# Optimization experiments

Hardware: AMD Instinct MI355X
Metric: run time of the kernel (lower is better)

The kernel has to match this reference:

```python
import jax, jax.numpy as jnp
import numpy as np
from jax import lax

E, S, Q, FEAT, HID, WAY = 4000, 25, 75, 64, 128, 5
ITERS = 10
LR = 0.01


def setup_inputs() -> dict:
    key = jax.random.key(0)
    ks = jax.random.split(key, 7)
    u = lambda k, shape, fan_in: jax.random.uniform(k, shape, jnp.float32, -1.0, 1.0) / jnp.sqrt(float(fan_in))
    return {
        "query_feat": jax.random.normal(ks[0], (E, Q, FEAT), jnp.float32),
        "support_feat": jax.random.normal(ks[1], (E, S, FEAT), jnp.float32),
        "support_targets": jax.random.randint(ks[2], (E, S), 0, WAY, jnp.int32),
        "W1": u(ks[3], (E, HID, FEAT), FEAT),
        "b1": u(ks[4], (E, HID), FEAT),
        "W2": u(ks[5], (E, WAY, HID), HID),
        "b2": u(ks[6], (E, WAY), HID),
    }


def _mlp(p, x):
    h = jax.nn.relu(x @ p["W1"].T + p["b1"])
    return h @ p["W2"].T + p["b2"]


def _train_episode(W1, b1, W2, b2, s_feat, s_tgt):
    params = {"W1": W1, "b1": b1, "W2": W2, "b2": b2}

    def loss_fn(p):
        logp = jax.nn.log_softmax(_mlp(p, s_feat), axis=-1)  # [S, WAY]
        return -jnp.mean(jnp.take_along_axis(logp, s_tgt[:, None], axis=1))

    def step(p, _):
        g = jax.grad(loss_fn)(p)
        return jax.tree.map(lambda a, b: a - LR * b, p, g), None

    params, _ = lax.scan(step, params, None, length=ITERS)
    return params


def reference(query_feat, support_feat, support_targets, W1, b1, W2, b2):
    # support features are detached in the original torch code
    support_feat = lax.stop_gradient(support_feat)

    def per_episode(q, s, t, w1, c1, w2, c2):
        p = _train_episode(w1, c1, w2, c2, s, t)
        return _mlp(p, q)  # [Q, WAY]

    out = jax.vmap(per_episode)(query_feat, support_feat, support_targets, W1, b1, W2, b2)
    return out.reshape(-1, out.shape[-1])  # torch.cat over episodes -> [E*Q, WAY]
```

## Files before the change

kernel.cpp:

```cpp
#include <hip/hip_runtime.h>

#define S 25
#define Q 75
#define FEAT 64
#define HID 128
#define WAY 5
#define NITERS 10
#define LR 0.01f
#define THREADS 256
#define HPAD 132

__device__ __forceinline__ int w1word(int j, int k) {
    const int q = k >> 2;
    return j * FEAT + ((q & 8) << 2) + (((q ^ j) & 7) << 2) + (k & 3);
}

__global__ __launch_bounds__(THREADS, 2)
void episode_kernel(const float* __restrict__ qf,
                    const float* __restrict__ sf,
                    const int* __restrict__ st,
                    const float* __restrict__ W1g,
                    const float* __restrict__ b1g,
                    const float* __restrict__ W2g,
                    const float* __restrict__ b2g,
                    float* __restrict__ outg)
{
    __shared__ __align__(16) float sW1[HID * FEAT];
    __shared__ __align__(16) float sW2[WAY * HID];
    __shared__ __align__(16) float sX[S * FEAT];
    __shared__ __align__(16) float sH[S * HPAD];
    __shared__ __align__(16) float sDh[S * HPAD];
    __shared__ __align__(16) float sDl[S * 8];
    __shared__ float sb1[HID];
    __shared__ float sb2[8];
    __shared__ int sTgt[S];

    const int e = blockIdx.x;
    const int t = threadIdx.x;

    const float* eQ  = qf  + (size_t)e * Q * FEAT;
    const float* eS  = sf  + (size_t)e * S * FEAT;
    const int*   eT  = st  + (size_t)e * S;
    const float* eW1 = W1g + (size_t)e * HID * FEAT;
    const float* eb1 = b1g + (size_t)e * HID;
    const float* eW2 = W2g + (size_t)e * WAY * HID;
    const float* eb2 = b2g + (size_t)e * WAY;
    float*       eO  = outg + (size_t)e * Q * WAY;

    for (int f = t; f < HID * FEAT; f += THREADS)
        sW1[w1word(f >> 6, f & 63)] = eW1[f];
    for (int f = t; f < S * FEAT; f += THREADS) sX[f] = eS[f];
    for (int f = t; f < WAY * HID; f += THREADS) sW2[f] = eW2[f];
    if (t < HID) sb1[t] = eb1[t];
    if (t < WAY) sb2[t] = eb2[t];
    if (t < S)   sTgt[t] = eT[t];
    __syncthreads();

    const int j   = t & (HID - 1);
    const int grp = t >> 7;
    const int i0  = grp * 12;
    const int jl = t & 63;
    const int k0 = (t >> 6) << 4;

    for (int iter = 0; iter < NITERS; ++iter) {
        {
            float acc[13];
            const float bv = sb1[j];
            #pragma unroll
            for (int r = 0; r < 13; ++r) acc[r] = bv;
            for (int qd = 0; qd < 16; ++qd) {
                const float4 w = *(const float4*)&sW1[j * FEAT + ((qd & 8) << 2) + (((qd ^ j) & 7) << 2)];
                const float* xp = &sX[i0 * FEAT + (qd << 2)];
                #pragma unroll
                for (int r = 0; r < 13; ++r) {
                    const float4 s = *(const float4*)&xp[r * FEAT];
                    acc[r] = fmaf(w.x, s.x, acc[r]);
                    acc[r] = fmaf(w.y, s.y, acc[r]);
                    acc[r] = fmaf(w.z, s.z, acc[r]);
                    acc[r] = fmaf(w.w, s.w, acc[r]);
                }
            }
            #pragma unroll
            for (int r = 0; r < 13; ++r) sH[(i0 + r) * HPAD + j] = fmaxf(acc[r], 0.f);
        }
        __syncthreads();

        if (t < S * WAY) {
            const int i = t / WAY;
            const int w = t - i * WAY;
            const float* hr = &sH[i * HPAD];
            const float* wr = &sW2[w * HID];
            float a = sb2[w];
            for (int qd = 0; qd < 32; ++qd) {
                const float4 hv = *(const float4*)&hr[qd << 2];
                const float4 wv = *(const float4*)&wr[qd << 2];
                a += hv.x * wv.x + hv.y * wv.y + hv.z * wv.z + hv.w * wv.w;
            }
            sDl[i * 8 + w] = a;
        }
        __syncthreads();

        if (t < S) {
            const float l0 = sDl[t*8+0], l1 = sDl[t*8+1], l2 = sDl[t*8+2],
                        l3 = sDl[t*8+3], l4 = sDl[t*8+4];
            const float m = fmaxf(fmaxf(fmaxf(l0, l1), fmaxf(l2, l3)), l4);
            const float e0 = __expf(l0 - m), e1 = __expf(l1 - m), e2 = __expf(l2 - m),
                        e3 = __expf(l3 - m), e4 = __expf(l4 - m);
            const float inv = 1.f / (e0 + e1 + e2 + e3 + e4);
            const int tg = sTgt[t];
            const float sc = 1.f / (float)S;
            sDl[t*8+0] = (e0 * inv - (tg == 0 ? 1.f : 0.f)) * sc;
            sDl[t*8+1] = (e1 * inv - (tg == 1 ? 1.f : 0.f)) * sc;
            sDl[t*8+2] = (e2 * inv - (tg == 2 ? 1.f : 0.f)) * sc;
            sDl[t*8+3] = (e3 * inv - (tg == 3 ? 1.f : 0.f)) * sc;
            sDl[t*8+4] = (e4 * inv - (tg == 4 ? 1.f : 0.f)) * sc;
        }
        __syncthreads();

        {
            const float w2v0 = sW2[0*HID + j], w2v1 = sW2[1*HID + j], w2v2 = sW2[2*HID + j],
                        w2v3 = sW2[3*HID + j], w2v4 = sW2[4*HID + j];
            #pragma unroll
            for (int r = 0; r < 13; ++r) {
                const int i = i0 + r;
                const float hv = sH[i * HPAD + j];
                const float4 d4 = *(const float4*)&sDl[i * 8];
                const float d5 = sDl[i * 8 + 4];
                const float d = d4.x * w2v0 + d4.y * w2v1 + d4.z * w2v2 + d4.w * w2v3 + d5 * w2v4;
                sDh[i * HPAD + j] = (hv > 0.f) ? d : 0.f;
            }
        }
        float gw20 = 0.f, gw21 = 0.f, gw22 = 0.f, gw23 = 0.f, gw24 = 0.f, gb2v = 0.f;
        if (t < HID) {
            for (int i = 0; i < S; ++i) {
                const float hv = sH[i * HPAD + t];
                const float4 d4 = *(const float4*)&sDl[i * 8];
                const float d5 = sDl[i * 8 + 4];
                gw20 = fmaf(d4.x, hv, gw20);
                gw21 = fmaf(d4.y, hv, gw21);
                gw22 = fmaf(d4.z, hv, gw22);
                gw23 = fmaf(d4.w, hv, gw23);
                gw24 = fmaf(d5, hv, gw24);
            }
        }
        if (t < WAY) {
            for (int i = 0; i < S; ++i) gb2v += sDl[i * 8 + t];
        }
        __syncthreads();

        if (t < HID) {
            sW2[0*HID + t] -= LR * gw20;
            sW2[1*HID + t] -= LR * gw21;
            sW2[2*HID + t] -= LR * gw22;
            sW2[3*HID + t] -= LR * gw23;
            sW2[4*HID + t] -= LR * gw24;
        }
        if (t < WAY) sb2[t] -= LR * gb2v;

        {
            float a0[16], a1[16];
            #pragma unroll
            for (int c = 0; c < 16; ++c) { a0[c] = 0.f; a1[c] = 0.f; }
            for (int i = 0; i < S; ++i) {
                const float d0 = sDh[i * HPAD + jl];
                const float d1 = sDh[i * HPAD + 64 + jl];
                const float* xp = &sX[i * FEAT + k0];
                float xv[16];
                *(float4*)&xv[0]  = *(const float4*)&xp[0];
                *(float4*)&xv[4]  = *(const float4*)&xp[4];
                *(float4*)&xv[8]  = *(const float4*)&xp[8];
                *(float4*)&xv[12] = *(const float4*)&xp[12];
                #pragma unroll
                for (int c = 0; c < 16; ++c) {
                    a0[c] = fmaf(d0, xv[c], a0[c]);
                    a1[c] = fmaf(d1, xv[c], a1[c]);
                }
            }
            #pragma unroll
            for (int c = 0; c < 16; ++c) {
                sW1[w1word(jl,      k0 + c)] -= LR * a0[c];
                sW1[w1word(jl + 64, k0 + c)] -= LR * a1[c];
            }
        }
        if (t < HID) {
            float g = 0.f;
            for (int i = 0; i < S; ++i) g += sDh[i * HPAD + t];
            sb1[t] -= LR * g;
        }
        __syncthreads();
    }

    for (int qc = 0; qc < 3; ++qc) {
        for (int f = t; f < S * FEAT; f += THREADS) sX[f] = eQ[qc * S * FEAT + f];
        __syncthreads();
        {
            float acc[13];
            const float bv = sb1[j];
            #pragma unroll
            for (int r = 0; r < 13; ++r) acc[r] = bv;
            for (int qd = 0; qd < 16; ++qd) {
                const float4 w = *(const float4*)&sW1[j * FEAT + ((qd & 8) << 2) + (((qd ^ j) & 7) << 2)];
                const float* xp = &sX[i0 * FEAT + (qd << 2)];
                #pragma unroll
                for (int r = 0; r < 13; ++r) {
                    const float4 s = *(const float4*)&xp[r * FEAT];
                    acc[r] = fmaf(w.x, s.x, acc[r]);
                    acc[r] = fmaf(w.y, s.y, acc[r]);
                    acc[r] = fmaf(w.z, s.z, acc[r]);
                    acc[r] = fmaf(w.w, s.w, acc[r]);
                }
            }
            #pragma unroll
            for (int r = 0; r < 13; ++r) sH[(i0 + r) * HPAD + j] = fmaxf(acc[r], 0.f);
        }
        __syncthreads();
        if (t < S * WAY) {
            const int i = t / WAY;
            const int w = t - i * WAY;
            const float* hr = &sH[i * HPAD];
            const float* wr = &sW2[w * HID];
            float a = sb2[w];
            for (int qd = 0; qd < 32; ++qd) {
                const float4 hv = *(const float4*)&hr[qd << 2];
                const float4 wv = *(const float4*)&wr[qd << 2];
                a += hv.x * wv.x + hv.y * wv.y + hv.z * wv.z + hv.w * wv.w;
            }
            eO[(qc * S + i) * WAY + w] = a;
        }
        __syncthreads();
    }
}

extern "C" void kernel_launch(void* const* d_in, const int* in_sizes, int n_in,
                              void* d_out, int out_size, void* d_ws, size_t ws_size,
                              hipStream_t stream) {
    const float* qf  = (const float*)d_in[0];
    const float* sf  = (const float*)d_in[1];
    const int*   st  = (const int*)d_in[2];
    const float* W1  = (const float*)d_in[3];
    const float* b1  = (const float*)d_in[4];
    const float* W2  = (const float*)d_in[5];
    const float* b2  = (const float*)d_in[6];
    float* out = (float*)d_out;
    const int n_eps = in_sizes[0] / (Q * FEAT);
    hipLaunchKernelGGL(episode_kernel, dim3(n_eps), dim3(THREADS), 0, stream,
                       qf, sf, st, W1, b1, W2, b2, out);
}
```

Measured before the change: 1.175 ms.

## Double block threads and redistribute per-episode work with shuffle-based softmax

Raises the block to 512 threads and remaps every phase to the wider block. The forward hidden pass now computes two hidden units by four rows per thread, and the W1 gradient uses eight features per thread with float4 read-modify-write updates. The logits and softmax phases are merged, with each row handled by an 8-lane group that uses xor-shuffle reductions, which removes one barrier. Global-to-shared loads are vectorised, and the W2/b2 gradient moves to otherwise idle threads. The aim is more parallel work and less per-thread serial work, at the cost of higher per-block thread count and an occupancy hint of 4 that may limit registers.

```diff
diff --git a/kernel.cpp b/kernel.cpp
--- a/kernel.cpp
+++ b/kernel.cpp
@@ -7,15 +7,14 @@
 #define WAY 5
 #define NITERS 10
 #define LR 0.01f
-#define THREADS 256
+#define THREADS 512
 #define HPAD 132
 
-__device__ __forceinline__ int w1word(int j, int k) {
-    const int q = k >> 2;
-    return j * FEAT + ((q & 8) << 2) + (((q ^ j) & 7) << 2) + (k & 3);
+__device__ __forceinline__ int w1q(int j, int q) {
+    return j * FEAT + ((q & 8) << 2) + (((q ^ j) & 7) << 2);
 }
 
-__global__ __launch_bounds__(THREADS, 2)
+__global__ __launch_bounds__(THREADS, 4)
 void episode_kernel(const float* __restrict__ qf,
                     const float* __restrict__ sf,
                     const int* __restrict__ st,
@@ -47,139 +46,188 @@
     const float* eb2 = b2g + (size_t)e * WAY;
     float*       eO  = outg + (size_t)e * Q * WAY;
 
-    for (int f = t; f < HID * FEAT; f += THREADS)
-        sW1[w1word(f >> 6, f & 63)] = eW1[f];
-    for (int f = t; f < S * FEAT; f += THREADS) sX[f] = eS[f];
-    for (int f = t; f < WAY * HID; f += THREADS) sW2[f] = eW2[f];
+    for (int f = t; f < HID * 16; f += THREADS) {
+        const int j = f >> 4, q = f & 15;
+        *(float4*)&sW1[w1q(j, q)] = *(const float4*)&eW1[f << 2];
+    }
+    for (int f = t; f < S * 16; f += THREADS)
+        *(float4*)&sX[f << 2] = *(const float4*)&eS[f << 2];
+    for (int f = t; f < WAY * 32; f += THREADS)
+        *(float4*)&sW2[f << 2] = *(const float4*)&eW2[f << 2];
     if (t < HID) sb1[t] = eb1[t];
     if (t < WAY) sb2[t] = eb2[t];
     if (t < S)   sTgt[t] = eT[t];
     __syncthreads();
 
-    const int j   = t & (HID - 1);
-    const int grp = t >> 7;
-    const int i0  = grp * 12;
-    const int jl = t & 63;
-    const int k0 = (t >> 6) << 4;
+    const int jl  = t & 63;
+    const int rg  = t >> 6;
+    const int i0f = rg * 4;
+    const int jd  = t & 127;
+    const int rg2 = t >> 7;
+    const int di0 = rg2 * 7;
+    const int jg = t & 63;
+    const int kb = t >> 6;
+    const int k0 = kb << 3;
+
+    auto fwd_hidden = [&]() {
+        float acc0[4], acc1[4];
+        const float bv0 = sb1[jl];
+        const float bv1 = sb1[jl + 64];
+        #pragma unroll
+        for (int r = 0; r < 4; ++r) { acc0[r] = bv0; acc1[r] = bv1; }
+        int irw[4];
+        #pragma unroll
+        for (int r = 0; r < 4; ++r) {
+            const int i = i0f + r;
+            irw[r] = (i < S ? i : S - 1) * FEAT;
+        }
+        #pragma unroll 4
+        for (int qd = 0; qd < 16; ++qd) {
+            const float4 w0 = *(const float4*)&sW1[w1q(jl, qd)];
+            const float4 w1 = *(const float4*)&sW1[w1q(jl + 64, qd)];
+            #pragma unroll
+            for (int r = 0; r < 4; ++r) {
+                const float4 xv = *(const float4*)&sX[irw[r] + (qd << 2)];
+                acc0[r] = fmaf(w0.x, xv.x, acc0[r]);
+                acc0[r] = fmaf(w0.y, xv.y, acc0[r]);
+                acc0[r] = fmaf(w0.z, xv.z, acc0[r]);
+                acc0[r] = fmaf(w0.w, xv.w, acc0[r]);
+                acc1[r] = fmaf(w1.x, xv.x, acc1[r]);
+                acc1[r] = fmaf(w1.y, xv.y, acc1[r]);
+                acc1[r] = fmaf(w1.z, xv.z, acc1[r]);
+                acc1[r] = fmaf(w1.w, xv.w, acc1[r]);
+            }
+        }
+        #pragma unroll
+        for (int r = 0; r < 4; ++r) {
+            const int i = i0f + r;
+            if (i < S) {
+                sH[i * HPAD + jl]      = fmaxf(acc0[r], 0.f);
+                sH[i * HPAD + jl + 64] = fmaxf(acc1[r], 0.f);
+            }
+        }
+    };
 
     for (int iter = 0; iter < NITERS; ++iter) {
+        fwd_hidden();
+        __syncthreads();
+
+        if (t < 200) {
+            const int li = t >> 3, lw = t & 7;
+            float a = -3.0e38f;
+            if (lw < WAY) {
+                const float* hr = &sH[li * HPAD];
+                const float* wr = &sW2[lw * HID];
+                a = sb2[lw];
+                #pragma unroll 8
+                for (int qd = 0; qd < 32; ++qd) {
+                    const float4 hv = *(const float4*)&hr[qd << 2];
+                    const float4 wv = *(const float4*)&wr[qd << 2];
+                    a += hv.x * wv.x + hv.y * wv.y + hv.z * wv.z + hv.w * wv.w;
+                }
+            }
+            float m = a;
+            #pragma unroll
+            for (int d = 1; d < 8; d <<= 1) m = fmaxf(m, __shfl_xor(m, d, 8));
+            const float ev = (lw < WAY) ? __expf(a - m) : 0.f;
+            float sum = ev;
+            #pragma unroll
+            for (int d = 1; d < 8; d <<= 1) sum += __shfl_xor(sum, d, 8);
+            if (lw < WAY) {
+                const float p = ev / sum;
+                sDl[li * 8 + lw] = (p - (sTgt[li] == lw ? 1.f : 0.f)) * (1.f / (float)S);
+            }
+        }
+        __syncthreads();
+
         {
-            float acc[13];
-            const float bv = sb1[j];
-            #pragma unroll
-            for (int r = 0; r < 13; ++r) acc[r] = bv;
-            for (int qd = 0; qd < 16; ++qd) {
-                const float4 w = *(const float4*)&sW1[j * FEAT + ((qd & 8) << 2) + (((qd ^ j) & 7) << 2)];
-                const float* xp = &sX[i0 * FEAT + (qd << 2)];
-                #pragma unroll
-                for (int r = 0; r < 13; ++r) {
-                    const float4 s = *(const float4*)&xp[r * FEAT];
-                    acc[r] = fmaf(w.x, s.x, acc[r]);
-                    acc[r] = fmaf(w.y, s.y, acc[r]);
-                    acc[r] = fmaf(w.z, s.z, acc[r]);
-                    acc[r] = fmaf(w.w, s.w, acc[r]);
+            const float w20 = sW2[0 * HID + jd], w21 = sW2[1 * HID + jd],
+                        w22 = sW2[2 * HID + jd], w23 = sW2[3 * HID + jd],
+                        w24 = sW2[4 * HID + jd];
+            #pragma unroll
+            for (int r = 0; r < 7; ++r) {
+                const int i = di0 + r;
+                if (i < S) {
+                    const float hv = sH[i * HPAD + jd];
+                    const float4 d4 = *(const float4*)&sDl[i * 8];
+                    const float d5 = sDl[i * 8 + 4];
+                    const float d = d4.x * w20 + d4.y * w21 + d4.z * w22 + d4.w * w23 + d5 * w24;
+                    sDh[i * HPAD + jd] = (hv > 0.f) ? d : 0.f;
                 }
             }
-            #pragma unroll
-            for (int r = 0; r < 13; ++r) sH[(i0 + r) * HPAD + j] = fmaxf(acc[r], 0.f);
-        }
-        __syncthreads();
-
-        if (t < S * WAY) {
-            const int i = t / WAY;
-            const int w = t - i * WAY;
-            const float* hr = &sH[i * HPAD];
-            const float* wr = &sW2[w * HID];
-            float a = sb2[w];
-            for (int qd = 0; qd < 32; ++qd) {
-                const float4 hv = *(const float4*)&hr[qd << 2];
-                const float4 wv = *(const float4*)&wr[qd << 2];
-                a += hv.x * wv.x + hv.y * wv.y + hv.z * wv.z + hv.w * wv.w;
-            }
-            sDl[i * 8 + w] = a;
-        }
-        __syncthreads();
-
-        if (t < S) {
-            const float l0 = sDl[t*8+0], l1 = sDl[t*8+1], l2 = sDl[t*8+2],
-                        l3 = sDl[t*8+3], l4 = sDl[t*8+4];
-            const float m = fmaxf(fmaxf(fmaxf(l0, l1), fmaxf(l2, l3)), l4);
-            const float e0 = __expf(l0 - m), e1 = __expf(l1 - m), e2 = __expf(l2 - m),
-                        e3 = __expf(l3 - m), e4 = __expf(l4 - m);
-            const float inv = 1.f / (e0 + e1 + e2 + e3 + e4);
-            const int tg = sTgt[t];
-            const float sc = 1.f / (float)S;
-            sDl[t*8+0] = (e0 * inv - (tg == 0 ? 1.f : 0.f)) * sc;
-            sDl[t*8+1] = (e1 * inv - (tg == 1 ? 1.f : 0.f)) * sc;
-            sDl[t*8+2] = (e2 * inv - (tg == 2 ? 1.f : 0.f)) * sc;
-            sDl[t*8+3] = (e3 * inv - (tg == 3 ? 1.f : 0.f)) * sc;
-            sDl[t*8+4] = (e4 * inv - (tg == 4 ? 1.f : 0.f)) * sc;
-        }
-        __syncthreads();
-
-        {
-            const float w2v0 = sW2[0*HID + j], w2v1 = sW2[1*HID + j], w2v2 = sW2[2*HID + j],
-                        w2v3 = sW2[3*HID + j], w2v4 = sW2[4*HID + j];
-            #pragma unroll
-            for (int r = 0; r < 13; ++r) {
-                const int i = i0 + r;
-                const float hv = sH[i * HPAD + j];
+        }
+        float gw2a0 = 0.f, gw2a1 = 0.f, gw2a2 = 0.f, gw2a3 = 0.f, gw2a4 = 0.f;
+        if (t >= 384) {
+            const int j2 = t - 384;
+            for (int i = 0; i < S; ++i) {
+                const float hv = sH[i * HPAD + j2];
                 const float4 d4 = *(const float4*)&sDl[i * 8];
                 const float d5 = sDl[i * 8 + 4];
-                const float d = d4.x * w2v0 + d4.y * w2v1 + d4.z * w2v2 + d4.w * w2v3 + d5 * w2v4;
-                sDh[i * HPAD + j] = (hv > 0.f) ? d : 0.f;
-            }
-        }
-        float gw20 = 0.f, gw21 = 0.f, gw22 = 0.f, gw23 = 0.f, gw24 = 0.f, gb2v = 0.f;
-        if (t < HID) {
+                gw2a0 = fmaf(d4.x, hv, gw2a0);
+                gw2a1 = fmaf(d4.y, hv, gw2a1);
+                gw2a2 = fmaf(d4.z, hv, gw2a2);
+                gw2a3 = fmaf(d4.w, hv, gw2a3);
+                gw2a4 = fmaf(d5, hv, gw2a4);
+            }
+        }
+        float gb2a = 0.f;
+        if (t >= 320 && t < 320 + WAY) {
+            for (int i = 0; i < S; ++i) gb2a += sDl[i * 8 + (t - 320)];
+        }
+        __syncthreads();
+
+        if (t >= 384) {
+            const int j2 = t - 384;
+            sW2[0 * HID + j2] -= LR * gw2a0;
+            sW2[1 * HID + j2] -= LR * gw2a1;
+            sW2[2 * HID + j2] -= LR * gw2a2;
+            sW2[3 * HID + j2] -= LR * gw2a3;
+            sW2[4 * HID + j2] -= LR * gw2a4;
+        }
+        if (t >= 320 && t < 320 + WAY) sb2[t - 320] -= LR * gb2a;
+        {
+            float a0[8], a1[8];
+            #pragma unroll
+            for (int c = 0; c < 8; ++c) { a0[c] = 0.f; a1[c] = 0.f; }
+            #pragma unroll 5
             for (int i = 0; i < S; ++i) {
-                const float hv = sH[i * HPAD + t];
-                const float4 d4 = *(const float4*)&sDl[i * 8];
-                const float d5 = sDl[i * 8 + 4];
-                gw20 = fmaf(d4.x, hv, gw20);
-                gw21 = fmaf(d4.y, hv, gw21);
-                gw22 = fmaf(d4.z, hv, gw22);
-                gw23 = fmaf(d4.w, hv, gw23);
-                gw24 = fmaf(d5, hv, gw24);
-            }
-        }
-        if (t < WAY) {
-            for (int i = 0; i < S; ++i) gb2v += sDl[i * 8 + t];
-        }
-        __syncthreads();
-
-        if (t < HID) {
-            sW2[0*HID + t] -= LR * gw20;
-            sW2[1*HID + t] -= LR * gw21;
-            sW2[2*HID + t] -= LR * gw22;
-            sW2[3*HID + t] -= LR * gw23;
-            sW2[4*HID + t] -= LR * gw24;
-        }
-        if (t < WAY) sb2[t] -= LR * gb2v;
-
-        {
-            float a0[16], a1[16];
-            #pragma unroll
-            for (int c = 0; c < 16; ++c) { a0[c] = 0.f; a1[c] = 0.f; }
-            for (int i = 0; i < S; ++i) {
-                const float d0 = sDh[i * HPAD + jl];
-                const float d1 = sDh[i * HPAD + 64 + jl];
-                const float* xp = &sX[i * FEAT + k0];
-                float xv[16];
-                *(float4*)&xv[0]  = *(const float4*)&xp[0];
-                *(float4*)&xv[4]  = *(const float4*)&xp[4];
-                *(float4*)&xv[8]  = *(const float4*)&xp[8];
-                *(float4*)&xv[12] = *(const float4*)&xp[12];
-                #pragma unroll
-                for (int c = 0; c < 16; ++c) {
-                    a0[c] = fmaf(d0, xv[c], a0[c]);
-                    a1[c] = fmaf(d1, xv[c], a1[c]);
-                }
-            }
-            #pragma unroll
-            for (int c = 0; c < 16; ++c) {
-                sW1[w1word(jl,      k0 + c)] -= LR * a0[c];
-                sW1[w1word(jl + 64, k0 + c)] -= LR * a1[c];
+                const float d0 = sDh[i * HPAD + jg];
+                const float d1 = sDh[i * HPAD + 64 + jg];
+                const float4 x0 = *(const float4*)&sX[i * FEAT + k0];
+                const float4 x1 = *(const float4*)&sX[i * FEAT + k0 + 4];
+                a0[0] = fmaf(d0, x0.x, a0[0]); a0[1] = fmaf(d0, x0.y, a0[1]);
+                a0[2] = fmaf(d0, x0.z, a0[2]); a0[3] = fmaf(d0, x0.w, a0[3]);
+                a0[4] = fmaf(d0, x1.x, a0[4]); a0[5] = fmaf(d0, x1.y, a0[5]);
+                a0[6] = fmaf(d0, x1.z, a0[6]); a0[7] = fmaf(d0, x1.w, a0[7]);
+                a1[0] = fmaf(d1, x0.x, a1[0]); a1[1] = fmaf(d1, x0.y, a1[1]);
+                a1[2] = fmaf(d1, x0.z, a1[2]); a1[3] = fmaf(d1, x0.w, a1[3]);
+                a1[4] = fmaf(d1, x1.x, a1[4]); a1[5] = fmaf(d1, x1.y, a1[5]);
+                a1[6] = fmaf(d1, x1.z, a1[6]); a1[7] = fmaf(d1, x1.w, a1[7]);
+            }
+            const int q0 = kb << 1, q1 = q0 + 1;
+            {
+                float4* p = (float4*)&sW1[w1q(jg, q0)];
+                float4 v = *p;
+                v.x -= LR * a0[0]; v.y -= LR * a0[1]; v.z -= LR * a0[2]; v.w -= LR * a0[3];
+                *p = v;
+            }
+            {
+                float4* p = (float4*)&sW1[w1q(jg, q1)];
+                float4 v = *p;
+                v.x -= LR * a0[4]; v.y -= LR * a0[5]; v.z -= LR * a0[6]; v.w -= LR * a0[7];
+                *p = v;
+            }
+            {
+                float4* p = (float4*)&sW1[w1q(jg + 64, q0)];
+                float4 v = *p;
+                v.x -= LR * a1[0]; v.y -= LR * a1[1]; v.z -= LR * a1[2]; v.w -= LR * a1[3];
+                *p = v;
+            }
+            {
+                float4* p = (float4*)&sW1[w1q(jg + 64, q1)];
+                float4 v = *p;
+                v.x -= LR * a1[4]; v.y -= LR * a1[5]; v.z -= LR * a1[6]; v.w -= LR * a1[7];
+                *p = v;
             }
         }
         if (t < HID) {
@@ -191,41 +239,25 @@
     }
 
     for (int qc = 0; qc < 3; ++qc) {
-        for (int f = t; f < S * FEAT; f += THREADS) sX[f] = eQ[qc * S * FEAT + f];
-        __syncthreads();
-        {
-            float acc[13];
-            const float bv = sb1[j];
-            #pragma unroll
-            for (int r = 0; r < 13; ++r) acc[r] = bv;
-            for (int qd = 0; qd < 16; ++qd) {
-                const float4 w = *(const float4*)&sW1[j * FEAT + ((qd & 8) << 2) + (((qd ^ j) & 7) << 2)];
-                const float* xp = &sX[i0 * FEAT + (qd << 2)];
-                #pragma unroll
-                for (int r = 0; r < 13; ++r) {
-                    const float4 s = *(const float4*)&xp[r * FEAT];
-                    acc[r] = fmaf(w.x, s.x, acc[r]);
-                    acc[r] = fmaf(w.y, s.y, acc[r]);
-                    acc[r] = fmaf(w.z, s.z, acc[r]);
-                    acc[r] = fmaf(w.w, s.w, acc[r]);
+        for (int f = t; f < S * 16; f += THREADS)
+            *(float4*)&sX[f << 2] = *(const float4*)&eQ[qc * (S * FEAT) + (f << 2)];
+        __syncthreads();
+        fwd_hidden();
+        __syncthreads();
+        if (t < 200) {
+            const int li = t >> 3, lw = t & 7;
+            if (lw < WAY) {
+                const float* hr = &sH[li * HPAD];
+                const float* wr = &sW2[lw * HID];
+                float a = sb2[lw];
+                #pragma unroll 8
+                for (int qd = 0; qd < 32; ++qd) {
+                    const float4 hv = *(const float4*)&hr[qd << 2];
+                    const float4 wv = *(const float4*)&wr[qd << 2];
+                    a += hv.x * wv.x + hv.y * wv.y + hv.z * wv.z + hv.w * wv.w;
                 }
-            }
-            #pragma unroll
-            for (int r = 0; r < 13; ++r) sH[(i0 + r) * HPAD + j] = fmaxf(acc[r], 0.f);
-        }
-        __syncthreads();
-        if (t < S * WAY) {
-            const int i = t / WAY;
-            const int w = t - i * WAY;
-            const float* hr = &sH[i * HPAD];
-            const float* wr = &sW2[w * HID];
-            float a = sb2[w];
-            for (int qd = 0; qd < 32; ++qd) {
-                const float4 hv = *(const float4*)&hr[qd << 2];
-                const float4 wv = *(const float4*)&wr[qd << 2];
-                a += hv.x * wv.x + hv.y * wv.y + hv.z * wv.z + hv.w * wv.w;
-            }
-            eO[(qc * S + i) * WAY + w] = a;
+                eO[(qc * S + li) * WAY + lw] = a;
+            }
         }
         __syncthreads();
     }
```

After: 1.133 ms. -3.5%, faster.
